# Performance work log

Hardware: AMD Instinct MI355X
Metric: run time of the kernel (lower is better)

## Reference

```python
import jax, jax.numpy as jnp
import numpy as np

M, IN, OUT, R = 8192, 4096, 4096, 16  # tokens, in_features, out_features, lora rank


def setup_inputs() -> dict:
    key = jax.random.key(0)
    k = jax.random.split(key, 7)
    # symmetric int8 quantized activations and weights
    x = jax.random.randint(k[0], (M, IN), -127, 128, dtype=jnp.int8)
    weight = jax.random.randint(k[1], (OUT, IN), -127, 128, dtype=jnp.int8)
    # per-token activation scales and per-output-channel weight scales
    x_scales = jax.random.uniform(k[2], (M,), jnp.float32, 0.5, 1.5) / 127.0
    scales = jax.random.uniform(k[3], (OUT,), jnp.float32, 0.5, 1.5) / 127.0
    bias = jax.random.normal(k[4], (OUT,), jnp.float32)
    # module inits lora_a ~ N(0, 1/r); lora_b is zeros in the module but we use
    # small random values so the LoRA path is numerically exercised
    lora_a = jax.random.normal(k[5], (R, IN), jnp.float32) * (1.0 / R)
    lora_b = jax.random.normal(k[6], (OUT, R), jnp.float32) * 0.02
    return dict(x=x, weight=weight, bias=bias, x_scales=x_scales,
                scales=scales, lora_a=lora_a, lora_b=lora_b, fuse_gelu=1)


def reference(x, weight, bias, x_scales, scales, lora_a, lora_b, fuse_gelu):
    acc = jax.lax.dot_general(x, weight, (((1,), (1,)), ((), ())),
                              preferred_element_type=jnp.int32)
    # dequantize with outer product of per-token and per-channel scales
    main = acc.astype(jnp.float32) * x_scales[:, None] * scales[None, :]
    # LoRA correction on the dequantized activations: (x_deq @ A^T) @ B^T
    x_deq = x.astype(jnp.float32) * x_scales[:, None]          # [M, IN]
    lora = (x_deq @ lora_a.T) @ lora_b.T                        # [M, R] @ [R, OUT]
    out = main + lora + bias[None, :]
    if fuse_gelu:  # static Python flag
        out = jax.nn.gelu(out, approximate=True)  # tanh-approx GELU (CUDA fused path)
    return out
```

## Files before the change

### kernel.cpp

```cpp
#include <hip/hip_runtime.h>

#define M_DIM 8192
#define IN_DIM 4096
#define OUT_DIM 4096

typedef int   v4i  __attribute__((ext_vector_type(4)));
typedef int   v16i __attribute__((ext_vector_type(16)));
typedef short v8s  __attribute__((ext_vector_type(8)));
typedef float v4f  __attribute__((ext_vector_type(4)));
typedef float v16f __attribute__((ext_vector_type(16)));

static __device__ __forceinline__ int pack4(int a, int b, int c, int d) {
    return (a & 255) | ((b & 255) << 8) | ((c & 255) << 16) | ((d & 255) << 24);
}

static __device__ __forceinline__ short f2bf(float f) {
    unsigned u = __float_as_uint(f);
    u = (u + 0x7FFFu + ((u >> 16) & 1u)) >> 16;
    return (short)u;
}

static __device__ __forceinline__ short i2bf(int v) {
    float f = (float)v;
    return (short)(__float_as_uint(f) >> 16);
}

static __device__ __forceinline__ float gelu_tanh(float u) {
    float u2 = u * u;
    float p  = fmaf(u2, 0.0356774081f, 0.7978845608f);
    float v  = u * p;
    float e  = __builtin_amdgcn_exp2f(v * 2.8853900818f);
    return u - u * __builtin_amdgcn_rcpf(e + 1.0f);
}

static __device__ __forceinline__ void async_cp16(const signed char* g, signed char* l) {
    __builtin_amdgcn_global_load_lds((const __attribute__((address_space(1))) void*)g,
                                     (__attribute__((address_space(3))) void*)l, 16, 0, 0);
}


__global__ __launch_bounds__(256) void pack_a_kernel(const float* __restrict__ la,
                                                     short* __restrict__ a16) {
    size_t i = ((size_t)blockIdx.x * 256 + threadIdx.x) * 8;
    const float4* p = (const float4*)(la + i);
    float4 a = p[0], b = p[1];
    v8s o;
    o[0] = f2bf(a.x); o[1] = f2bf(a.y); o[2] = f2bf(a.z); o[3] = f2bf(a.w);
    o[4] = f2bf(b.x); o[5] = f2bf(b.y); o[6] = f2bf(b.z); o[7] = f2bf(b.w);
    *(v8s*)(a16 + i) = o;
}

__global__ __launch_bounds__(256) void pack_w_kernel(const int* __restrict__ w,
                                                     signed char* __restrict__ w8t) {
    const int flat = blockIdx.x * 256 + threadIdx.x;
    const int l  = flat & 63;
    const int gp = (flat >> 6) & 15;
    const int kk = (flat >> 10) & 63;
    const int bn = flat >> 16;
    const int n = bn * 256 + ((gp >> 1) << 5) + (l & 31);
    const int k = kk * 64 + ((gp & 1) << 5) + ((l >> 5) << 4);
    const int4* p = (const int4*)(w + (size_t)n * IN_DIM + k);
    int4 a = p[0], b = p[1], c = p[2], d = p[3];
    int4 o;
    o.x = pack4(a.x, a.y, a.z, a.w);
    o.y = pack4(b.x, b.y, b.z, b.w);
    o.z = pack4(c.x, c.y, c.z, c.w);
    o.w = pack4(d.x, d.y, d.z, d.w);
    *(int4*)(w8t + (size_t)flat * 16) = o;
}

__global__ __launch_bounds__(256) void pack_x_lora_kernel(const int* __restrict__ x,
                                                          const short* __restrict__ a16,
                                                          signed char* __restrict__ x8t,
                                                          float* __restrict__ T) {
    __shared__ float red[4 * 256];
    const int tid = threadIdx.x;
    const int lane = tid & 63, wv = tid >> 6;
    const int fr = lane & 15, fq = lane >> 4;
    const int m0 = blockIdx.x * 16;
    const int bm = m0 >> 8;
    const int g  = (m0 >> 5) & 7;
    const int l5 = (m0 & 16) + fr;
    const int row = m0 + fr;

    v4f acc = {0.f, 0.f, 0.f, 0.f};
#pragma unroll 2
    for (int kt = 0; kt < 32; ++kt) {
        const int k  = wv * 1024 + kt * 32 + fq * 8;
        const int4* xp = (const int4*)(x + (size_t)row * IN_DIM + k);
        int4 a = xp[0], b = xp[1];
        const int kk = k >> 6, c = (k >> 4) & 3, j8 = (k >> 3) & 1;
        int2 pk = make_int2(pack4(a.x, a.y, a.z, a.w), pack4(b.x, b.y, b.z, b.w));
        *(int2*)(x8t + ((size_t)((bm * 64 + kk) * 16 + g * 2 + (c >> 1))) * 1024 +
                 ((c & 1) * 32 + l5) * 16 + j8 * 8) = pk;
        v8s xa;
        xa[0] = i2bf(a.x); xa[1] = i2bf(a.y); xa[2] = i2bf(a.z); xa[3] = i2bf(a.w);
        xa[4] = i2bf(b.x); xa[5] = i2bf(b.y); xa[6] = i2bf(b.z); xa[7] = i2bf(b.w);
        v8s aa = *(const v8s*)(a16 + (size_t)fr * IN_DIM + k);
        acc = __builtin_amdgcn_mfma_f32_16x16x32_bf16(xa, aa, acc, 0, 0, 0);
    }
    *(v4f*)&red[wv * 256 + lane * 4] = acc;
    __syncthreads();

    float s = red[tid] + red[256 + tid] + red[512 + tid] + red[768 + tid];
    const int sl = tid >> 2, j = tid & 3;
    const int r16 = ((sl >> 4) << 2) + j, col = sl & 15;
    T[(size_t)(m0 + r16) * 16 + col] = s;
}

__global__ __launch_bounds__(256, 1) void q8_gemm_kernel(
    const signed char* __restrict__ x8t, const signed char* __restrict__ w8t,
    const float* __restrict__ Tp, const float* __restrict__ lbm,
    const float* __restrict__ bias, const float* __restrict__ xsc,
    const float* __restrict__ wsc, const int* __restrict__ gflag,
    float* __restrict__ out) {
    __shared__ __align__(16) signed char smem[65536];

    const int tid  = threadIdx.x;
    const int lane = tid & 63;
    const int wv   = tid >> 6;
    const int wm   = wv >> 1, wn = wv & 1;
    const int b   = blockIdx.x;
    const int xcd = b & 7, rr = b >> 3;
    const int bm  = xcd * 4 + (rr & 3);
    const int bn  = rr >> 2;

    const int lofs = lane * 16;
    const signed char* Asrc = x8t + (size_t)bm * (64 * 16 * 1024);
    const signed char* Bsrc = w8t + (size_t)bn * (64 * 16 * 1024);
    signed char* ldsA = smem + wv * 4096;
    signed char* ldsB = smem + 16384 + wv * 4096;

    v16i acc[4][4];
    {
        v16i z;
#pragma unroll
        for (int i = 0; i < 16; ++i) z[i] = 0;
#pragma unroll
        for (int mt = 0; mt < 4; ++mt)
#pragma unroll
            for (int nt = 0; nt < 4; ++nt) acc[mt][nt] = z;
    }

    {
        const signed char* as = Asrc + (size_t)(wv * 4) * 1024 + lofs;
        const signed char* bs = Bsrc + (size_t)(wv * 4) * 1024 + lofs;
#pragma unroll
        for (int i = 0; i < 4; ++i) {
            async_cp16(as + i * 1024, ldsA + i * 1024);
            async_cp16(bs + i * 1024, ldsB + i * 1024);
        }
    }

    for (int kk = 0; kk < 64; ++kk) {
        __syncthreads();
        if (kk + 1 < 64) {
            const int nb = (kk + 1) & 1;
            const signed char* as = Asrc + ((size_t)(kk + 1) * 16 + wv * 4) * 1024 + lofs;
            const signed char* bs = Bsrc + ((size_t)(kk + 1) * 16 + wv * 4) * 1024 + lofs;
#pragma unroll
            for (int i = 0; i < 4; ++i) {
                async_cp16(as + i * 1024, ldsA + nb * 32768 + i * 1024);
                async_cp16(bs + i * 1024, ldsB + nb * 32768 + i * 1024);
            }
        }
        const signed char* Ab = smem + (kk & 1) * 32768;
        const signed char* Bb = Ab + 16384;
#pragma unroll
        for (int s = 0; s < 2; ++s) {
            v4i av[4], bv[4];
#pragma unroll
            for (int mt = 0; mt < 4; ++mt)
                av[mt] = *(const v4i*)(Ab + ((wm * 4 + mt) * 2 + s) * 1024 + lofs);
#pragma unroll
            for (int nt = 0; nt < 4; ++nt)
                bv[nt] = *(const v4i*)(Bb + ((wn * 4 + nt) * 2 + s) * 1024 + lofs);
#pragma unroll
            for (int mt = 0; mt < 4; ++mt)
#pragma unroll
                for (int nt = 0; nt < 4; ++nt)
                    acc[mt][nt] = __builtin_amdgcn_mfma_i32_32x32x32_i8(
                        av[mt], bv[nt], acc[mt][nt], 0, 0, 0);
        }
    }

    const int mbase = bm * 256 + wm * 128;
    const int nbase = bn * 256 + wn * 128;
    const int l31 = lane & 31, lh = lane >> 5;
    const bool dg = (*gflag) != 0;

    v8s tf[4], bf[4];
#pragma unroll
    for (int mt = 0; mt < 4; ++mt) {
        const float* t0 = Tp + (size_t)(mbase + mt * 32 + l31) * 16 + lh * 8;
        v8s v;
#pragma unroll
        for (int j = 0; j < 8; ++j) v[j] = f2bf(t0[j]);
        tf[mt] = v;
    }
#pragma unroll
    for (int nt = 0; nt < 4; ++nt) {
        const float* bp = lbm + (size_t)(nbase + nt * 32 + l31) * 16 + lh * 8;
        v8s v;
#pragma unroll
        for (int j = 0; j < 8; ++j) v[j] = f2bf(bp[j]);
        bf[nt] = v;
    }
    float wsa[4], bba[4];
#pragma unroll
    for (int nt = 0; nt < 4; ++nt) {
        const int col = nbase + nt * 32 + l31;
        wsa[nt] = wsc[col];
        bba[nt] = bias[col];
    }

#pragma unroll
    for (int mt = 0; mt < 4; ++mt) {
        const int rowb = mbase + mt * 32 + lh * 4;
        float4 xs0 = *(const float4*)(xsc + rowb);
        float4 xs1 = *(const float4*)(xsc + rowb + 8);
        float4 xs2 = *(const float4*)(xsc + rowb + 16);
        float4 xs3 = *(const float4*)(xsc + rowb + 24);
        float xsv[16] = {xs0.x, xs0.y, xs0.z, xs0.w, xs1.x, xs1.y, xs1.z, xs1.w,
                         xs2.x, xs2.y, xs2.z, xs2.w, xs3.x, xs3.y, xs3.z, xs3.w};
#pragma unroll
        for (int nt = 0; nt < 4; ++nt) {
            v16f fa;
#pragma unroll
            for (int i = 0; i < 16; ++i) fa[i] = (float)acc[mt][nt][i] * wsa[nt];
            fa = __builtin_amdgcn_mfma_f32_32x32x16_bf16(tf[mt], bf[nt], fa, 0, 0, 0);
            const int col = nbase + nt * 32 + l31;
#pragma unroll
            for (int r = 0; r < 16; ++r) {
                float u = fmaf(xsv[r], fa[r], bba[nt]);
                if (dg) u = gelu_tanh(u);
                out[(size_t)(rowb + (r & 3) + 8 * (r >> 2)) * OUT_DIM + col] = u;
            }
        }
    }
}

extern "C" void kernel_launch(void* const* d_in, const int* in_sizes, int n_in,
                              void* d_out, int out_size, void* d_ws, size_t ws_size,
                              hipStream_t stream) {
    const int*   x     = (const int*)d_in[0];
    const int*   wt    = (const int*)d_in[1];
    const float* bias  = (const float*)d_in[2];
    const float* xsc   = (const float*)d_in[3];
    const float* wsc   = (const float*)d_in[4];
    const float* la    = (const float*)d_in[5];
    const float* lb    = (const float*)d_in[6];
    const int*   gflag = (const int*)d_in[7];
    float* out = (float*)d_out;

    signed char* x8t = (signed char*)d_ws;
    signed char* w8t = x8t + (size_t)M_DIM * IN_DIM;
    float* T = (float*)(w8t + (size_t)OUT_DIM * IN_DIM);
    short* a16 = (short*)w8t;

    pack_a_kernel<<<16 * IN_DIM / (8 * 256), 256, 0, stream>>>(la, a16);
    pack_x_lora_kernel<<<M_DIM / 16, 256, 0, stream>>>(x, a16, x8t, T);
    pack_w_kernel<<<(size_t)OUT_DIM * IN_DIM / (16 * 256), 256, 0, stream>>>(wt, w8t);
    q8_gemm_kernel<<<(M_DIM / 256) * (OUT_DIM / 256), 256, 0, stream>>>(
        x8t, w8t, T, lb, bias, xsc, wsc, gflag, out);
}
```

Before: 442.9 us.

## Shrink GEMM block tile to 128x256 for two blocks per CU

```diff
diff --git a/kernel.cpp b/kernel.cpp
--- a/kernel.cpp
+++ b/kernel.cpp
@@ -108,75 +108,72 @@
     T[(size_t)(m0 + r16) * 16 + col] = s;
 }
 
-__global__ __launch_bounds__(256, 1) void q8_gemm_kernel(
+__global__ __launch_bounds__(256, 2) void q8_gemm_kernel(
     const signed char* __restrict__ x8t, const signed char* __restrict__ w8t,
     const float* __restrict__ Tp, const float* __restrict__ lbm,
     const float* __restrict__ bias, const float* __restrict__ xsc,
     const float* __restrict__ wsc, const int* __restrict__ gflag,
     float* __restrict__ out) {
-    __shared__ __align__(16) signed char smem[65536];
+    __shared__ __align__(16) signed char smem[49152];
 
     const int tid  = threadIdx.x;
     const int lane = tid & 63;
     const int wv   = tid >> 6;
     const int wm   = wv >> 1, wn = wv & 1;
     const int b   = blockIdx.x;
-    const int xcd = b & 7, rr = b >> 3;
-    const int bm  = xcd * 4 + (rr & 3);
-    const int bn  = rr >> 2;
+    const int xcd = b & 7, idx = b >> 3;
+    const int bm  = xcd * 8 + (idx & 7);
+    const int bn  = idx >> 3;
 
     const int lofs = lane * 16;
-    const signed char* Asrc = x8t + (size_t)bm * (64 * 16 * 1024);
-    const signed char* Bsrc = w8t + (size_t)bn * (64 * 16 * 1024);
-    signed char* ldsA = smem + wv * 4096;
-    signed char* ldsB = smem + 16384 + wv * 4096;
-
-    v16i acc[4][4];
+    const signed char* Abase = x8t + (size_t)(bm >> 1) * (64 * 16 * 1024) + (bm & 1) * 8192;
+    const signed char* Bbase = w8t + (size_t)bn * (64 * 16 * 1024);
+
+    v16i acc[2][4];
     {
         v16i z;
 #pragma unroll
         for (int i = 0; i < 16; ++i) z[i] = 0;
 #pragma unroll
-        for (int mt = 0; mt < 4; ++mt)
+        for (int mt = 0; mt < 2; ++mt)
 #pragma unroll
             for (int nt = 0; nt < 4; ++nt) acc[mt][nt] = z;
     }
 
-    {
-        const signed char* as = Asrc + (size_t)(wv * 4) * 1024 + lofs;
-        const signed char* bs = Bsrc + (size_t)(wv * 4) * 1024 + lofs;
-#pragma unroll
-        for (int i = 0; i < 4; ++i) {
-            async_cp16(as + i * 1024, ldsA + i * 1024);
-            async_cp16(bs + i * 1024, ldsB + i * 1024);
-        }
+#pragma unroll
+    for (int i = 0; i < 6; ++i) {
+        const int c = wv * 6 + i;
+        const signed char* src = (c < 8) ? (Abase + (size_t)c * 1024 + lofs)
+                                         : (Bbase + (size_t)(c - 8) * 1024 + lofs);
+        async_cp16(src, smem + c * 1024);
     }
 
     for (int kk = 0; kk < 64; ++kk) {
         __syncthreads();
         if (kk + 1 < 64) {
             const int nb = (kk + 1) & 1;
-            const signed char* as = Asrc + ((size_t)(kk + 1) * 16 + wv * 4) * 1024 + lofs;
-            const signed char* bs = Bsrc + ((size_t)(kk + 1) * 16 + wv * 4) * 1024 + lofs;
-#pragma unroll
-            for (int i = 0; i < 4; ++i) {
-                async_cp16(as + i * 1024, ldsA + nb * 32768 + i * 1024);
-                async_cp16(bs + i * 1024, ldsB + nb * 32768 + i * 1024);
+            const size_t ko = (size_t)(kk + 1) * 16 * 1024;
+#pragma unroll
+            for (int i = 0; i < 6; ++i) {
+                const int c = wv * 6 + i;
+                const signed char* src = (c < 8) ? (Abase + ko + (size_t)c * 1024 + lofs)
+                                                 : (Bbase + ko + (size_t)(c - 8) * 1024 + lofs);
+                async_cp16(src, smem + nb * 24576 + c * 1024);
             }
         }
-        const signed char* Ab = smem + (kk & 1) * 32768;
-        const signed char* Bb = Ab + 16384;
+        const signed char* Ab = smem + (kk & 1) * 24576;
+        const signed char* Bb = Ab + 8192;
 #pragma unroll
         for (int s = 0; s < 2; ++s) {
-            v4i av[4], bv[4];
-#pragma unroll
-            for (int mt = 0; mt < 4; ++mt)
-                av[mt] = *(const v4i*)(Ab + ((wm * 4 + mt) * 2 + s) * 1024 + lofs);
+            v4i av[2], bv[4];
+#pragma unroll
+            for (int mt = 0; mt < 2; ++mt)
+                av[mt] = *(const v4i*)(Ab + ((wm * 2 + mt) * 2 + s) * 1024 + lofs);
 #pragma unroll
             for (int nt = 0; nt < 4; ++nt)
                 bv[nt] = *(const v4i*)(Bb + ((wn * 4 + nt) * 2 + s) * 1024 + lofs);
 #pragma unroll
-            for (int mt = 0; mt < 4; ++mt)
+            for (int mt = 0; mt < 2; ++mt)
 #pragma unroll
                 for (int nt = 0; nt < 4; ++nt)
                     acc[mt][nt] = __builtin_amdgcn_mfma_i32_32x32x32_i8(
@@ -184,14 +181,14 @@
         }
     }
 
-    const int mbase = bm * 256 + wm * 128;
+    const int mbase = bm * 128 + wm * 64;
     const int nbase = bn * 256 + wn * 128;
     const int l31 = lane & 31, lh = lane >> 5;
     const bool dg = (*gflag) != 0;
 
-    v8s tf[4], bf[4];
-#pragma unroll
-    for (int mt = 0; mt < 4; ++mt) {
+    v8s tf[2], bf[4];
+#pragma unroll
+    for (int mt = 0; mt < 2; ++mt) {
         const float* t0 = Tp + (size_t)(mbase + mt * 32 + l31) * 16 + lh * 8;
         v8s v;
 #pragma unroll
@@ -215,7 +212,7 @@
     }
 
 #pragma unroll
-    for (int mt = 0; mt < 4; ++mt) {
+    for (int mt = 0; mt < 2; ++mt) {
         const int rowb = mbase + mt * 32 + lh * 4;
         float4 xs0 = *(const float4*)(xsc + rowb);
         float4 xs1 = *(const float4*)(xsc + rowb + 8);
@@ -261,6 +258,6 @@
     pack_a_kernel<<<16 * IN_DIM / (8 * 256), 256, 0, stream>>>(la, a16);
     pack_x_lora_kernel<<<M_DIM / 16, 256, 0, stream>>>(x, a16, x8t, T);
     pack_w_kernel<<<(size_t)OUT_DIM * IN_DIM / (16 * 256), 256, 0, stream>>>(wt, w8t);
-    q8_gemm_kernel<<<(M_DIM / 256) * (OUT_DIM / 256), 256, 0, stream>>>(
+    q8_gemm_kernel<<<(M_DIM / 128) * (OUT_DIM / 256), 256, 0, stream>>>(
         x8t, w8t, T, lb, bias, xsc, wsc, gflag, out);
 }
```

After: 444.8 us. About the same (+0.4%).
